# Kernel optimization log

Measured on AMD Instinct MI355X. Metric: run time of the kernel, lower is better.

Reference implementation:

```python
import jax, jax.numpy as jnp
import numpy as np

H = 1024      # hidden_size
NH = 16       # num_attention_heads
HD = H // NH  # attention_head_size = 64
FF = 4096     # intermediate_size
EPS = 1e-5


def setup_inputs() -> dict:
    key = jax.random.key(0)
    ks = jax.random.split(key, 16)
    B, S = 8, 512
    s = lambda d: 1.0 / np.sqrt(d)
    return {
        "hidden_states": jax.random.normal(ks[0], (B, S, H), jnp.float32),
        "attention_mask": jnp.zeros((B, 1, 1, S), jnp.float32),  # additive mask
        "wq": jax.random.normal(ks[1], (H, H), jnp.float32) * s(H),
        "bq": jnp.zeros((H,), jnp.float32),
        "wk": jax.random.normal(ks[2], (H, H), jnp.float32) * s(H),
        "bk": jnp.zeros((H,), jnp.float32),
        "wv": jax.random.normal(ks[3], (H, H), jnp.float32) * s(H),
        "bv": jnp.zeros((H,), jnp.float32),
        "wo": jax.random.normal(ks[4], (H, H), jnp.float32) * s(H),
        "bo": jnp.zeros((H,), jnp.float32),
        "ln1_g": jnp.ones((H,), jnp.float32),
        "ln1_b": jnp.zeros((H,), jnp.float32),
        "wi": jax.random.normal(ks[5], (H, FF), jnp.float32) * s(H),
        "bi": jnp.zeros((FF,), jnp.float32),
        "wo2": jax.random.normal(ks[6], (FF, H), jnp.float32) * s(FF),
        "bo2": jnp.zeros((H,), jnp.float32),
        "ln2_g": jnp.ones((H,), jnp.float32),
        "ln2_b": jnp.zeros((H,), jnp.float32),
    }


def _layer_norm(x, g, b):
    mu = jnp.mean(x, axis=-1, keepdims=True)
    var = jnp.mean(jnp.square(x - mu), axis=-1, keepdims=True)
    return (x - mu) * jax.lax.rsqrt(var + EPS) * g + b


def reference(hidden_states, attention_mask, wq, bq, wk, bk, wv, bv,
              wo, bo, ln1_g, ln1_b, wi, bi, wo2, bo2, ln2_g, ln2_b):
    B, S, _ = hidden_states.shape
    split = lambda x: x.reshape(B, S, NH, HD).transpose(0, 2, 1, 3)  # [B,NH,S,HD]
    q = split(hidden_states @ wq + bq)
    k = split(hidden_states @ wk + bk)
    v = split(hidden_states @ wv + bv)
    # scaled dot-product attention with additive mask (dropout = eval identity)
    scores = jnp.einsum("bhqd,bhkd->bhqk", q, k) / np.sqrt(HD)
    scores = scores + attention_mask
    probs = jax.nn.softmax(scores, axis=-1)
    ctx = jnp.einsum("bhqk,bhkd->bhqd", probs, v)
    ctx = ctx.transpose(0, 2, 1, 3).reshape(B, S, H)
    # RobertaSelfOutput: dense + residual + LayerNorm
    attn_out = _layer_norm(ctx @ wo + bo + hidden_states, ln1_g, ln1_b)
    # FFN: intermediate (gelu) + output dense + residual + LayerNorm
    inter = jax.nn.gelu(attn_out @ wi + bi, approximate=False)
    layer_out = _layer_norm(inter @ wo2 + bo2 + attn_out, ln2_g, ln2_b)
    return layer_out
```

## Files before the change

### kernel.cpp

```cpp
#include <hip/hip_runtime.h>
#include <math.h>

#define DI __device__ __forceinline__

typedef unsigned short u16;
typedef __attribute__((ext_vector_type(8))) u16 u16x8;
typedef __attribute__((ext_vector_type(4))) u16 u16x4;
typedef __attribute__((ext_vector_type(8))) __bf16 bf16x8;
typedef __attribute__((ext_vector_type(4))) float f32x4;

typedef const __attribute__((address_space(1))) unsigned int g_u32;
typedef __attribute__((address_space(3))) unsigned int l_u32;

DI float bf2f(u16 u) {
  unsigned v = ((unsigned)u) << 16;
  float f; __builtin_memcpy(&f, &v, 4); return f;
}
DI u16 f2bf(float f) {
  unsigned u; __builtin_memcpy(&u, &f, 4);
  u += 0x7fff + ((u >> 16) & 1);
  return (u16)(u >> 16);
}
DI f32x4 mfma16(bf16x8 a, bf16x8 b, f32x4 c) {
  return __builtin_amdgcn_mfma_f32_16x16x32_bf16(a, b, c, 0, 0, 0);
}
DI void gl16(const void* g, const u16* lds) {
  __builtin_amdgcn_global_load_lds((g_u32*)g, (l_u32*)lds, 16, 0, 0);
}
DI unsigned cvtpk(float lo, float hi) {
  unsigned d;
  asm("v_cvt_pk_bf16_f32 %0, %1, %2" : "=v"(d) : "v"(lo), "v"(hi));
  return d;
}

__global__ __launch_bounds__(256) void cvt_bf16_k(const float* __restrict__ in,
                                                  u16* __restrict__ out, int n) {
  int i = (blockIdx.x * 256 + threadIdx.x) * 8;
  if (i >= n) return;
  float4 a = *(const float4*)(in + i);
  float4 b = *(const float4*)(in + i + 4);
  u16x8 o;
  o[0] = f2bf(a.x); o[1] = f2bf(a.y); o[2] = f2bf(a.z); o[3] = f2bf(a.w);
  o[4] = f2bf(b.x); o[5] = f2bf(b.y); o[6] = f2bf(b.z); o[7] = f2bf(b.w);
  *(u16x8*)(out + i) = o;
}

__global__ __launch_bounds__(256) void tcvt_k(const float* __restrict__ in,
                                              u16* __restrict__ out, int K, int N) {
  __shared__ float tile[32][33];
  int n0 = blockIdx.x * 32, k0 = blockIdx.y * 32;
  int tx = threadIdx.x & 31, ty = threadIdx.x >> 5;
  #pragma unroll
  for (int i = 0; i < 4; i++) {
    int kr = ty + i * 8;
    tile[kr][tx] = in[(size_t)(k0 + kr) * N + n0 + tx];
  }
  __syncthreads();
  #pragma unroll
  for (int i = 0; i < 4; i++) {
    int nr = ty + i * 8;
    out[(size_t)(n0 + nr) * K + k0 + tx] = f2bf(tile[tx][nr]);
  }
}

__global__ __launch_bounds__(256) void pack_bias_k(const float* __restrict__ b0,
                                                   const float* __restrict__ b1,
                                                   const float* __restrict__ b2,
                                                   float* __restrict__ out) {
  int i = blockIdx.x * 256 + threadIdx.x;
  float v = (i < 1024) ? b0[i] : (i < 2048 ? b1[i - 1024] : b2[i - 2048]);
  out[i] = v;
}

__global__ __launch_bounds__(256) void vtr_k(const u16* __restrict__ QKV,
                                             u16* __restrict__ VT) {
  __shared__ u16 tile[64][72];
  const int t = threadIdx.x;
  const int kt = blockIdx.x, bh = blockIdx.y;
  const int b = bh >> 4, h = bh & 15;
  {
    int r = t >> 2, d0 = (t & 3) * 16;
    const u16* src = &QKV[((size_t)(b * 512 + kt * 64 + r)) * 3072 + 2048 + h * 64 + d0];
    *(u16x8*)&tile[r][d0] = *(const u16x8*)src;
    *(u16x8*)&tile[r][d0 + 8] = *(const u16x8*)(src + 8);
  }
  __syncthreads();
  int d = t >> 2, kseg = (t & 3) * 16;
  u16x8 o0, o1;
  #pragma unroll
  for (int j = 0; j < 8; j++) { o0[j] = tile[kseg + j][d]; o1[j] = tile[kseg + 8 + j][d]; }
  u16* dst = &VT[((size_t)bh << 15) + (size_t)d * 512 + kt * 64 + kseg];
  *(u16x8*)dst = o0;
  *(u16x8*)(dst + 8) = o1;
}

#define QUAD(d, mh, nh) do {                                                          \
  const u16* Ab_ = &sA[d][wr][0];                                                     \
  const u16* Bb_ = &sB[d][wc >> 1][0];                                                \
  bf16x8 af_[4][2], bv_[2][2];                                                        \
  _Pragma("unroll") for (int i_ = 0; i_ < 4; i_++) {                                  \
    int row_ = (mh) * 64 + i_ * 16 + r15;                                             \
    _Pragma("unroll") for (int ks_ = 0; ks_ < 2; ks_++)                               \
      af_[i_][ks_] = *(const bf16x8*)&Ab_[row_ * 64 + ((((ks_ << 2) | kg) + row_) & 7) * 8]; } \
  _Pragma("unroll") for (int j_ = 0; j_ < 2; j_++) {                                  \
    int row_ = (wc & 1) * 64 + (nh) * 32 + j_ * 16 + r15;                             \
    _Pragma("unroll") for (int ks_ = 0; ks_ < 2; ks_++)                               \
      bv_[j_][ks_] = *(const bf16x8*)&Bb_[row_ * 64 + ((((ks_ << 2) | kg) + row_) & 7) * 8]; } \
  __builtin_amdgcn_s_barrier();                                                       \
  __builtin_amdgcn_s_setprio(1);                                                      \
  _Pragma("unroll") for (int i_ = 0; i_ < 4; i_++)                                    \
    _Pragma("unroll") for (int j_ = 0; j_ < 2; j_++)                                  \
      _Pragma("unroll") for (int ks_ = 0; ks_ < 2; ks_++)                             \
        acc[(mh) * 4 + i_][(nh) * 2 + j_] =                                           \
            mfma16(af_[i_][ks_], bv_[j_][ks_], acc[(mh) * 4 + i_][(nh) * 2 + j_]);    \
  __builtin_amdgcn_s_setprio(0);                                                      \
} while (0)

template<int EPI, int SPLITK>
__global__ __launch_bounds__(512, 2) void gemm8p_k(const u16* __restrict__ A,
                                                   const u16* __restrict__ Bt,
                                                   const float* __restrict__ bias,
                                                   void* __restrict__ out,
                                                   int M, int N, int K) {
  __shared__ __align__(16) u16 sA[2][2][128 * 64];
  __shared__ __align__(16) u16 sB[2][2][128 * 64];
  const int tid = threadIdx.x;
  const int lane = tid & 63, wid = tid >> 6;
  const int wr = wid >> 2, wc = wid & 3;
  const int r15 = lane & 15, kg = lane >> 4;

  const int GX = gridDim.x, GY = gridDim.y;
  int nwg = GX * GY;
  int orig = blockIdx.y * GX + blockIdx.x;
  int s = (orig & 7) * (nwg >> 3) + (orig >> 3);
  int bx = s / GY, by = s - bx * GY;
  const int bm = by * 256, bn = bx * 256;

  const int z = blockIdx.z;
  int tilesK = K >> 6;
  int qs = tilesK / SPLITK, rs = tilesK - qs * SPLITK;
  int ntz = qs + (z < rs ? 1 : 0);
  int k0 = (z * qs + (z < rs ? z : rs)) << 6;

  f32x4 acc[8][4];
  #pragma unroll
  for (int i = 0; i < 8; i++)
    #pragma unroll
    for (int j = 0; j < 4; j++) acc[i][j] = (f32x4){0.f, 0.f, 0.f, 0.f};

  const int drw = tid >> 3;
  const int gsl8 = ((tid - drw) & 7) << 3;
  const u16* pA0 = A  + (size_t)(bm +       drw) * K + k0 + gsl8;
  const u16* pA1 = A  + (size_t)(bm + 128 + drw) * K + k0 + gsl8;
  const u16* pB0 = Bt + (size_t)(bn +       drw) * K + k0 + gsl8;
  const u16* pB1 = Bt + (size_t)(bn + 128 + drw) * K + k0 + gsl8;
  const size_t s2o = (size_t)64 * K;
  const int dld = wid << 9;

  auto stageTile = [&](int d) {
    u16* dA0 = &sA[d][0][dld]; u16* dA1 = &sA[d][1][dld];
    u16* dB0 = &sB[d][0][dld]; u16* dB1 = &sB[d][1][dld];
    gl16(pA0, dA0); gl16(pA0 + s2o, dA0 + 4096);
    gl16(pB0, dB0); gl16(pB0 + s2o, dB0 + 4096);
    gl16(pA1, dA1); gl16(pA1 + s2o, dA1 + 4096);
    gl16(pB1, dB1); gl16(pB1 + s2o, dB1 + 4096);
    pA0 += 64; pA1 += 64; pB0 += 64; pB1 += 64;
  };

  stageTile(0);
  if (ntz > 1) stageTile(1);

  for (int t = 0; t < ntz; ++t) {
    int d = t & 1;
    if (t + 1 < ntz) asm volatile("s_waitcnt vmcnt(8)" ::: "memory");
    else             asm volatile("s_waitcnt vmcnt(0)" ::: "memory");
    __builtin_amdgcn_s_barrier();
    QUAD(d, 0, 0);
    QUAD(d, 0, 1);
    QUAD(d, 1, 0);
    QUAD(d, 1, 1);
    __builtin_amdgcn_s_barrier();
    __builtin_amdgcn_sched_barrier(0);
    if (t + 2 < ntz) stageTile(d);
  }

  #pragma unroll
  for (int ii = 0; ii < 8; ii++) {
    int row = bm + wr * 128 + ii * 16 + kg * 4;
    #pragma unroll
    for (int jj = 0; jj < 4; jj++) {
      int col = bn + wc * 64 + jj * 16 + r15;
      if (EPI == 4) {
        size_t zoff = (size_t)z * M * N;
        #pragma unroll
        for (int q2 = 0; q2 < 4; q2++)
          ((float*)out)[zoff + (size_t)(row + q2) * N + col] = acc[ii][jj][q2];
      } else {
        float bv = bias[col];
        #pragma unroll
        for (int q2 = 0; q2 < 4; q2++) {
          float v = acc[ii][jj][q2] + bv;
          if (EPI == 2) v = 0.5f * v * (1.0f + erff(v * 0.70710678118f));
          ((u16*)out)[(size_t)(row + q2) * N + col] = f2bf(v);
        }
      }
    }
  }
}

template<int EPI>
__global__ __launch_bounds__(256) void gemm_bt_k(const u16* __restrict__ A,
                                                 const u16* __restrict__ Bt,
                                                 const float* __restrict__ bias,
                                                 const void* __restrict__ resid,
                                                 u16* __restrict__ out,
                                                 int M, int N, int K) {
  __shared__ __align__(16) u16 As[2][128 * 64];
  __shared__ __align__(16) u16 Bs[2][128 * 64];
  const int tid = threadIdx.x;
  const int lane = tid & 63, wid = tid >> 6;
  const int wm = (wid >> 1) * 64, wn = (wid & 1) * 64;
  const int r15 = lane & 15, kg = lane >> 4;
  const int srow = lane >> 3;

  const int GX = gridDim.x, GY = gridDim.y;
  int nwg = GX * GY;
  int orig = blockIdx.y * GX + blockIdx.x;
  int s = (orig & 7) * (nwg >> 3) + (orig >> 3);
  int bx = s / GY, by = s - bx * GY;
  const int bm = by * 128, bn = bx * 128;

  f32x4 acc[4][4];
  #pragma unroll
  for (int i = 0; i < 4; i++)
    #pragma unroll
    for (int j = 0; j < 4; j++) acc[i][j] = (f32x4){0.f, 0.f, 0.f, 0.f};

  const u16* pAc[4]; const u16* pBc[4];
  #pragma unroll
  for (int c = 0; c < 4; c++) {
    int chunk = (c << 2) | wid;
    int row = (chunk << 3) + srow;
    int gsl = ((lane & 7) - row) & 7;
    pAc[c] = A  + (size_t)(bm + row) * K + (gsl << 3);
    pBc[c] = Bt + (size_t)(bn + row) * K + (gsl << 3);
  }
  auto STAGE = [&](int buf, int kt) {
    #pragma unroll
    for (int c = 0; c < 4; c++) {
      int chunk = (c << 2) | wid;
      gl16(pAc[c] + kt, &As[buf][chunk << 9]);
      gl16(pBc[c] + kt, &Bs[buf][chunk << 9]);
    }
  };
  auto COMPUTE = [&](int buf) {
    #pragma unroll
    for (int ks = 0; ks < 2; ks++) {
      bf16x8 af[4], bfr[4];
      #pragma unroll
      for (int i = 0; i < 4; i++) {
        int row = wm + i * 16 + r15;
        af[i] = *(const bf16x8*)&As[buf][row * 64 + (((ks << 2) + kg + row) & 7) * 8];
      }
      #pragma unroll
      for (int i = 0; i < 4; i++) {
        int row = wn + i * 16 + r15;
        bfr[i] = *(const bf16x8*)&Bs[buf][row * 64 + (((ks << 2) + kg + row) & 7) * 8];
      }
      #pragma unroll
      for (int i = 0; i < 4; i++)
        #pragma unroll
        for (int j = 0; j < 4; j++)
          acc[i][j] = mfma16(af[i], bfr[j], acc[i][j]);
    }
  };

  const int nt = K >> 6;
  STAGE(0, 0);
  if (nt > 1) STAGE(1, 64);
  for (int t = 0; t < nt; ++t) {
    if (t + 1 < nt) asm volatile("s_waitcnt vmcnt(8)" ::: "memory");
    else            asm volatile("s_waitcnt vmcnt(0)" ::: "memory");
    __builtin_amdgcn_s_barrier();
    COMPUTE(t & 1);
    __builtin_amdgcn_s_barrier();
    __builtin_amdgcn_sched_barrier(0);
    if (t + 2 < nt) STAGE(t & 1, (t + 2) << 6);
  }

  #pragma unroll
  for (int i = 0; i < 4; i++) {
    int row0 = bm + wm + i * 16 + kg * 4;
    #pragma unroll
    for (int j = 0; j < 4; j++) {
      int col = bn + wn + j * 16 + r15;
      float bv = bias[col];
      #pragma unroll
      for (int q2 = 0; q2 < 4; q2++) {
        int row = row0 + q2;
        float v = acc[i][j][q2] + bv;
        if (EPI == 1) v += ((const float*)resid)[(size_t)row * N + col];
        out[(size_t)row * N + col] = f2bf(v);
      }
    }
  }
}

__global__ __launch_bounds__(256) void fattn_k(const u16* __restrict__ QKV,
                                               const u16* __restrict__ VT,
                                               const float* __restrict__ mask,
                                               u16* __restrict__ ctx) {
  __shared__ __align__(16) u16 sK[2][64 * 64];
  __shared__ __align__(16) u16 sV[2][64 * 64];
  __shared__ float sMask[512];
  const int t = threadIdx.x, lane = t & 63, wid = t >> 6;
  const int q15 = lane & 15, g = lane >> 4;
  const int qb = blockIdx.x, h = blockIdx.y, b = blockIdx.z;
  const int bh = b * 16 + h;
  const int qrow0 = qb * 128 + wid * 32;

  if (t < 128) *(float4*)&sMask[t * 4] = *(const float4*)&mask[b * 512 + t * 4];

  bf16x8 qf[2][2];
  #pragma unroll
  for (int qt = 0; qt < 2; qt++)
    #pragma unroll
    for (int c = 0; c < 2; c++)
      qf[qt][c] = *(const bf16x8*)&QKV[(size_t)(b * 512 + qrow0 + qt * 16 + q15) * 3072 +
                                       h * 64 + c * 32 + g * 8];

  const int srow0 = t >> 3;
  const int ssl = (((t & 7) - (t >> 3)) & 7) << 3;
  const u16* pK = QKV + (size_t)(b * 512 + srow0) * 3072 + 1024 + h * 64 + ssl;
  const u16* pV = VT + ((size_t)bh << 15) + (size_t)srow0 * 512 + ssl;
  const size_t kS2 = (size_t)32 * 3072;
  const size_t vS2 = (size_t)32 * 512;
  const int dld = t * 8;

  auto stage = [&](int d) {
    gl16(pK, &sK[d][dld]); gl16(pK + kS2, &sK[d][dld + 2048]);
    gl16(pV, &sV[d][dld]); gl16(pV + vS2, &sV[d][dld + 2048]);
    pK += 64 * 3072; pV += 64;
  };

  stage(0); stage(1);

  float m_[2] = {-1e30f, -1e30f}, l_[2] = {0.f, 0.f};
  f32x4 oacc[2][4];
  #pragma unroll
  for (int qt = 0; qt < 2; qt++)
    #pragma unroll
    for (int dt = 0; dt < 4; dt++) oacc[qt][dt] = (f32x4){0.f, 0.f, 0.f, 0.f};

  const int bp0 = ((g & 1) * 32 + q15) * 4;
  const int bp1 = bp0 + 64;

  for (int kt = 0; kt < 8; ++kt) {
    const int d = kt & 1;
    if (kt < 7) asm volatile("s_waitcnt vmcnt(4)" ::: "memory");
    else        asm volatile("s_waitcnt vmcnt(0)" ::: "memory");
    __builtin_amdgcn_s_barrier();

    f32x4 sc[2][4];
    #pragma unroll
    for (int qt = 0; qt < 2; qt++)
      #pragma unroll
      for (int k16 = 0; k16 < 4; k16++) sc[qt][k16] = (f32x4){0.f, 0.f, 0.f, 0.f};
    #pragma unroll
    for (int k16 = 0; k16 < 4; k16++) {
      int row = k16 * 16 + q15;
      bf16x8 ak0 = *(const bf16x8*)&sK[d][row * 64 + ((g + row) & 7) * 8];
      bf16x8 ak1 = *(const bf16x8*)&sK[d][row * 64 + ((4 + g + row) & 7) * 8];
      #pragma unroll
      for (int qt = 0; qt < 2; qt++) {
        sc[qt][k16] = mfma16(ak0, qf[qt][0], sc[qt][k16]);
        sc[qt][k16] = mfma16(ak1, qf[qt][1], sc[qt][k16]);
      }
    }

    float mk[4][4];
    #pragma unroll
    for (int k16 = 0; k16 < 4; k16++)
      #pragma unroll
      for (int r = 0; r < 4; r++)
        mk[k16][r] = sMask[kt * 64 + k16 * 16 + g * 4 + r];
    float p[2][16];
    #pragma unroll
    for (int qt = 0; qt < 2; qt++)
      #pragma unroll
      for (int k16 = 0; k16 < 4; k16++)
        #pragma unroll
        for (int r = 0; r < 4; r++)
          p[qt][k16 * 4 + r] = sc[qt][k16][r] * 0.125f + mk[k16][r];

    #pragma unroll
    for (int qt = 0; qt < 2; qt++) {
      float tmax = p[qt][0];
      #pragma unroll
      for (int j = 1; j < 16; j++) tmax = fmaxf(tmax, p[qt][j]);
      tmax = fmaxf(tmax, __shfl_xor(tmax, 16));
      tmax = fmaxf(tmax, __shfl_xor(tmax, 32));
      float mn = fmaxf(m_[qt], tmax);
      float al = __expf(m_[qt] - mn);
      m_[qt] = mn;
      float ts = 0.f;
      #pragma unroll
      for (int j = 0; j < 16; j++) { p[qt][j] = __expf(p[qt][j] - mn); ts += p[qt][j]; }
      ts += __shfl_xor(ts, 16);
      ts += __shfl_xor(ts, 32);
      l_[qt] = l_[qt] * al + ts;
      #pragma unroll
      for (int r = 0; r < 4; r++) {
        float alq = __shfl(al, g * 4 + r);
        #pragma unroll
        for (int dt = 0; dt < 4; dt++) oacc[qt][dt][r] *= alq;
      }
    }

    unsigned dwp[2][4][2];
    #pragma unroll
    for (int qt = 0; qt < 2; qt++)
      #pragma unroll
      for (int k16 = 0; k16 < 4; k16++) {
        dwp[qt][k16][0] = cvtpk(p[qt][k16 * 4 + 0], p[qt][k16 * 4 + 1]);
        dwp[qt][k16][1] = cvtpk(p[qt][k16 * 4 + 2], p[qt][k16 * 4 + 3]);
      }

    #pragma unroll
    for (int cp = 0; cp < 2; cp++) {
      bf16x8 pa[2];
      #pragma unroll
      for (int qt = 0; qt < 2; qt++) {
        union { unsigned u[4]; bf16x8 v; } pu;
        #pragma unroll
        for (int pp = 0; pp < 2; pp++) {
          unsigned a0 = __builtin_amdgcn_ds_bpermute(bp0, (int)dwp[qt][2 * cp][pp]);
          unsigned b0 = __builtin_amdgcn_ds_bpermute(bp0, (int)dwp[qt][2 * cp + 1][pp]);
          unsigned a1 = __builtin_amdgcn_ds_bpermute(bp1, (int)dwp[qt][2 * cp][pp]);
          unsigned b1 = __builtin_amdgcn_ds_bpermute(bp1, (int)dwp[qt][2 * cp + 1][pp]);
          pu.u[pp] = (g & 2) ? b0 : a0;
          pu.u[2 + pp] = (g & 2) ? b1 : a1;
        }
        pa[qt] = pu.v;
      }
      #pragma unroll
      for (int dt = 0; dt < 4; dt++) {
        int row = dt * 16 + q15;
        bf16x8 vf = *(const bf16x8*)&sV[d][row * 64 + (((cp << 2) + g + row) & 7) * 8];
        oacc[0][dt] = mfma16(pa[0], vf, oacc[0][dt]);
        oacc[1][dt] = mfma16(pa[1], vf, oacc[1][dt]);
      }
    }

    __builtin_amdgcn_s_barrier();
    __builtin_amdgcn_sched_barrier(0);
    if (kt + 2 < 8) stage(d);
  }

  #pragma unroll
  for (int qt = 0; qt < 2; qt++) {
    float linv[4];
    #pragma unroll
    for (int r = 0; r < 4; r++) linv[r] = 1.0f / __shfl(l_[qt], g * 4 + r);
    #pragma unroll
    for (int dt = 0; dt < 4; dt++)
      #pragma unroll
      for (int r = 0; r < 4; r++) {
        int row = qrow0 + qt * 16 + g * 4 + r;
        ctx[(size_t)(b * 512 + row) * 1024 + h * 64 + dt * 16 + q15] =
            f2bf(oacc[qt][dt][r] * linv[r]);
      }
  }
}

template<int OUTF32>
__global__ __launch_bounds__(256) void ln_k(const u16* __restrict__ in,
                                            const float* __restrict__ g,
                                            const float* __restrict__ be,
                                            void* __restrict__ out) {
  int row = blockIdx.x, t = threadIdx.x;
  const u16* rp = in + (size_t)row * 1024 + t * 4;
  u16x4 raw = *(const u16x4*)rp;
  float x[4];
  #pragma unroll
  for (int i = 0; i < 4; i++) x[i] = bf2f(raw[i]);
  float s = x[0] + x[1] + x[2] + x[3];
  float q = x[0]*x[0] + x[1]*x[1] + x[2]*x[2] + x[3]*x[3];
  #pragma unroll
  for (int off = 32; off; off >>= 1) {
    s += __shfl_down(s, off);
    q += __shfl_down(q, off);
  }
  __shared__ float rs_[4], rq_[4];
  int wid = t >> 6, lane = t & 63;
  if (!lane) { rs_[wid] = s; rq_[wid] = q; }
  __syncthreads();
  float S1 = rs_[0] + rs_[1] + rs_[2] + rs_[3];
  float S2 = rq_[0] + rq_[1] + rq_[2] + rq_[3];
  float mu = S1 * (1.0f / 1024.0f);
  float inv = rsqrtf(S2 * (1.0f / 1024.0f) - mu * mu + 1e-5f);
  #pragma unroll
  for (int i = 0; i < 4; i++) {
    int c = t * 4 + i;
    float y = (x[i] - mu) * inv * g[c] + be[c];
    if (OUTF32) ((float*)out)[(size_t)row * 1024 + c] = y;
    else        ((u16*)out)[(size_t)row * 1024 + c] = f2bf(y);
  }
}

__global__ __launch_bounds__(256) void ln2r_k(const float* __restrict__ part,
                                              const float* __restrict__ bias,
                                              const u16* __restrict__ resid,
                                              const float* __restrict__ g,
                                              const float* __restrict__ be,
                                              float* __restrict__ out) {
  const int row = blockIdx.x, t = threadIdx.x;
  const size_t base = (size_t)row * 1024 + t * 4;
  float4 p0 = *(const float4*)(part + base);
  float4 p1 = *(const float4*)(part + 4194304 + base);
  float4 p2 = *(const float4*)(part + 8388608 + base);
  u16x4 rr = *(const u16x4*)(resid + base);
  float x[4];
  x[0] = p0.x + p1.x + p2.x + bias[t*4+0] + bf2f(rr[0]);
  x[1] = p0.y + p1.y + p2.y + bias[t*4+1] + bf2f(rr[1]);
  x[2] = p0.z + p1.z + p2.z + bias[t*4+2] + bf2f(rr[2]);
  x[3] = p0.w + p1.w + p2.w + bias[t*4+3] + bf2f(rr[3]);
  float s = x[0] + x[1] + x[2] + x[3];
  float q = x[0]*x[0] + x[1]*x[1] + x[2]*x[2] + x[3]*x[3];
  #pragma unroll
  for (int off = 32; off; off >>= 1) {
    s += __shfl_down(s, off);
    q += __shfl_down(q, off);
  }
  __shared__ float rs_[4], rq_[4];
  int wid = t >> 6, lane = t & 63;
  if (!lane) { rs_[wid] = s; rq_[wid] = q; }
  __syncthreads();
  float S1 = rs_[0] + rs_[1] + rs_[2] + rs_[3];
  float S2 = rq_[0] + rq_[1] + rq_[2] + rq_[3];
  float mu = S1 * (1.0f / 1024.0f);
  float inv = rsqrtf(S2 * (1.0f / 1024.0f) - mu * mu + 1e-5f);
  #pragma unroll
  for (int i = 0; i < 4; i++) {
    int c = t * 4 + i;
    out[(size_t)row * 1024 + c] = (x[i] - mu) * inv * g[c] + be[c];
  }
}

extern "C" void kernel_launch(void* const* d_in, const int* in_sizes, int n_in,
                              void* d_out, int out_size, void* d_ws, size_t ws_size,
                              hipStream_t stream) {
  const float* hidden = (const float*)d_in[0];
  const float* mask   = (const float*)d_in[1];
  const float* wq  = (const float*)d_in[2];  const float* bq  = (const float*)d_in[3];
  const float* wk  = (const float*)d_in[4];  const float* bk  = (const float*)d_in[5];
  const float* wv  = (const float*)d_in[6];  const float* bv  = (const float*)d_in[7];
  const float* wo  = (const float*)d_in[8];  const float* bo  = (const float*)d_in[9];
  const float* ln1g = (const float*)d_in[10]; const float* ln1b = (const float*)d_in[11];
  const float* wi  = (const float*)d_in[12]; const float* bi  = (const float*)d_in[13];
  const float* wo2 = (const float*)d_in[14]; const float* bo2 = (const float*)d_in[15];
  const float* ln2g = (const float*)d_in[16]; const float* ln2b = (const float*)d_in[17];

  char* ws = (char*)d_ws;
  u16*   WqkvT = (u16*)(ws + 0);
  u16*   WoT   = (u16*)(ws + 6291456);
  u16*   Xb    = (u16*)(ws + 8388608);
  u16*   VTb   = (u16*)(ws + 8388608);
  u16*   QKVb  = (u16*)(ws + 16777216);
  u16*   Ctx   = (u16*)(ws + 41943040);
  u16*   AD    = (u16*)(ws + 50331648);
  float* part  = (float*)(ws + 0);
  u16*   AO    = (u16*)(ws + 58720256);
  u16*   Inter = (u16*)(ws + 67108864);
  u16*   WiT   = (u16*)(ws + 100663296);
  u16*   Wo2T  = (u16*)(ws + 109051904);
  float* bqkv  = (float*)(ws + 117440512);

  cvt_bf16_k<<<2048, 256, 0, stream>>>(hidden, Xb, 4194304);
  tcvt_k<<<dim3(32, 32),  256, 0, stream>>>(wq,  WqkvT,                1024, 1024);
  tcvt_k<<<dim3(32, 32),  256, 0, stream>>>(wk,  WqkvT + 1024 * 1024,  1024, 1024);
  tcvt_k<<<dim3(32, 32),  256, 0, stream>>>(wv,  WqkvT + 2048 * 1024,  1024, 1024);
  tcvt_k<<<dim3(32, 32),  256, 0, stream>>>(wo,  WoT,  1024, 1024);
  tcvt_k<<<dim3(128, 32), 256, 0, stream>>>(wi,  WiT,  1024, 4096);
  tcvt_k<<<dim3(32, 128), 256, 0, stream>>>(wo2, Wo2T, 4096, 1024);
  pack_bias_k<<<12, 256, 0, stream>>>(bq, bk, bv, bqkv);

  gemm8p_k<0, 1><<<dim3(12, 16, 1), 512, 0, stream>>>(Xb, WqkvT, bqkv, QKVb, 4096, 3072, 1024);

  vtr_k<<<dim3(8, 128), 256, 0, stream>>>(QKVb, VTb);

  fattn_k<<<dim3(4, 16, 8), 256, 0, stream>>>(QKVb, VTb, mask, Ctx);

  gemm_bt_k<1><<<dim3(8, 32), 256, 0, stream>>>(Ctx, WoT, bo, hidden, AD, 4096, 1024, 1024);
  ln_k<0><<<4096, 256, 0, stream>>>(AD, ln1g, ln1b, AO);

  gemm8p_k<2, 1><<<dim3(16, 16, 1), 512, 0, stream>>>(AO, WiT, bi, Inter, 4096, 4096, 1024);

  gemm8p_k<4, 3><<<dim3(4, 16, 3), 512, 0, stream>>>(Inter, Wo2T, nullptr, part, 4096, 1024, 4096);

  ln2r_k<<<4096, 256, 0, stream>>>(part, bo2, AO, ln2g, ln2b, (float*)d_out);
}
```

Before: 374.2 us.

## Interleave per-half global prefetch with MFMA phases in 256x256 GEMM

Restructures the 8-wave GEMM main loop so each wave computes a checkerboard of A/B halves. The global-to-LDS loads for the next k-tile are issued in four quarter-tile chunks, interleaved between the four MFMA phases with finer vmcnt waits. This replaces the old whole-tile double-buffer refill at the end of each iteration. It also changes the warp-to-output mapping so A fragments can be reused across phases, which cuts LDS reads. The intent is better overlap of memory traffic with matrix math, at the cost of more barriers and tighter waitcnt ordering that could introduce hazards.

After: 388.2 us. +3.7%, slower.

```diff
diff --git a/kernel.cpp b/kernel.cpp
--- a/kernel.cpp
+++ b/kernel.cpp
@@ -94,25 +94,24 @@
   *(u16x8*)(dst + 8) = o1;
 }
 
-#define QUAD(d, mh, nh) do {                                                          \
-  const u16* Ab_ = &sA[d][wr][0];                                                     \
-  const u16* Bb_ = &sB[d][wc >> 1][0];                                                \
-  bf16x8 af_[4][2], bv_[2][2];                                                        \
+#define LD_A(half) do { const u16* Ah_ = &sA[d][half][0];                             \
   _Pragma("unroll") for (int i_ = 0; i_ < 4; i_++) {                                  \
-    int row_ = (mh) * 64 + i_ * 16 + r15;                                             \
+    int row_ = wr * 64 + i_ * 16 + r15;                                               \
     _Pragma("unroll") for (int ks_ = 0; ks_ < 2; ks_++)                               \
-      af_[i_][ks_] = *(const bf16x8*)&Ab_[row_ * 64 + ((((ks_ << 2) | kg) + row_) & 7) * 8]; } \
+      afr[i_][ks_] = *(const bf16x8*)&Ah_[row_ * 64 + (((ks_ * 4 + kg) + row_) & 7) * 8]; } \
+} while (0)
+#define LD_B(half) do { const u16* Bh_ = &sB[d][half][0];                             \
   _Pragma("unroll") for (int j_ = 0; j_ < 2; j_++) {                                  \
-    int row_ = (wc & 1) * 64 + (nh) * 32 + j_ * 16 + r15;                             \
+    int row_ = wc * 32 + j_ * 16 + r15;                                               \
     _Pragma("unroll") for (int ks_ = 0; ks_ < 2; ks_++)                               \
-      bv_[j_][ks_] = *(const bf16x8*)&Bb_[row_ * 64 + ((((ks_ << 2) | kg) + row_) & 7) * 8]; } \
-  __builtin_amdgcn_s_barrier();                                                       \
-  __builtin_amdgcn_s_setprio(1);                                                      \
+      bvr[j_][ks_] = *(const bf16x8*)&Bh_[row_ * 64 + (((ks_ * 4 + kg) + row_) & 7) * 8]; } \
+} while (0)
+#define MFMA_PH(ah, bh) do { __builtin_amdgcn_s_setprio(1);                           \
   _Pragma("unroll") for (int i_ = 0; i_ < 4; i_++)                                    \
     _Pragma("unroll") for (int j_ = 0; j_ < 2; j_++)                                  \
       _Pragma("unroll") for (int ks_ = 0; ks_ < 2; ks_++)                             \
-        acc[(mh) * 4 + i_][(nh) * 2 + j_] =                                           \
-            mfma16(af_[i_][ks_], bv_[j_][ks_], acc[(mh) * 4 + i_][(nh) * 2 + j_]);    \
+        acc[(ah) * 4 + i_][(bh) * 2 + j_] =                                           \
+            mfma16(afr[i_][ks_], bvr[j_][ks_], acc[(ah) * 4 + i_][(bh) * 2 + j_]);    \
   __builtin_amdgcn_s_setprio(0);                                                      \
 } while (0)
 
@@ -157,55 +156,67 @@
   const size_t s2o = (size_t)64 * K;
   const int dld = wid << 9;
 
-  auto stageTile = [&](int d) {
-    u16* dA0 = &sA[d][0][dld]; u16* dA1 = &sA[d][1][dld];
-    u16* dB0 = &sB[d][0][dld]; u16* dB1 = &sB[d][1][dld];
-    gl16(pA0, dA0); gl16(pA0 + s2o, dA0 + 4096);
-    gl16(pB0, dB0); gl16(pB0 + s2o, dB0 + 4096);
-    gl16(pA1, dA1); gl16(pA1 + s2o, dA1 + 4096);
-    gl16(pB1, dB1); gl16(pB1 + s2o, dB1 + 4096);
-    pA0 += 64; pA1 += 64; pB0 += 64; pB1 += 64;
-  };
-
-  stageTile(0);
-  if (ntz > 1) stageTile(1);
+  auto stA0 = [&](int d) { u16* D = &sA[d][0][dld]; gl16(pA0, D); gl16(pA0 + s2o, D + 4096); pA0 += 64; };
+  auto stB0 = [&](int d) { u16* D = &sB[d][0][dld]; gl16(pB0, D); gl16(pB0 + s2o, D + 4096); pB0 += 64; };
+  auto stA1 = [&](int d) { u16* D = &sA[d][1][dld]; gl16(pA1, D); gl16(pA1 + s2o, D + 4096); pA1 += 64; };
+  auto stB1 = [&](int d) { u16* D = &sB[d][1][dld]; gl16(pB1, D); gl16(pB1 + s2o, D + 4096); pB1 += 64; };
+
+  stA0(0); stB0(0); stA1(0); stB1(0);
 
   for (int t = 0; t < ntz; ++t) {
-    int d = t & 1;
-    if (t + 1 < ntz) asm volatile("s_waitcnt vmcnt(8)" ::: "memory");
-    else             asm volatile("s_waitcnt vmcnt(0)" ::: "memory");
+    const int d = t & 1;
+    const bool pf = (t + 1 < ntz);
+    bf16x8 afr[4][2], bvr[2][2];
+
+    asm volatile("s_waitcnt vmcnt(4)" ::: "memory");
+    asm volatile("s_waitcnt lgkmcnt(0)" ::: "memory");
+    __builtin_amdgcn_sched_barrier(0);
     __builtin_amdgcn_s_barrier();
-    QUAD(d, 0, 0);
-    QUAD(d, 0, 1);
-    QUAD(d, 1, 0);
-    QUAD(d, 1, 1);
+    if (pf) stA0(d ^ 1);
+    LD_A(0); LD_B(0);
+    MFMA_PH(0, 0);
+    if (pf) { asm volatile("s_waitcnt vmcnt(4)" ::: "memory"); stB0(d ^ 1); }
+    else    { asm volatile("s_waitcnt vmcnt(2)" ::: "memory"); }
     __builtin_amdgcn_s_barrier();
-    __builtin_amdgcn_sched_barrier(0);
-    if (t + 2 < ntz) stageTile(d);
-  }
-
-  #pragma unroll
-  for (int ii = 0; ii < 8; ii++) {
-    int row = bm + wr * 128 + ii * 16 + kg * 4;
-    #pragma unroll
-    for (int jj = 0; jj < 4; jj++) {
-      int col = bn + wc * 64 + jj * 16 + r15;
-      if (EPI == 4) {
-        size_t zoff = (size_t)z * M * N;
+    LD_A(1);
+    MFMA_PH(1, 0);
+    if (pf) { asm volatile("s_waitcnt vmcnt(4)" ::: "memory"); stA1(d ^ 1); }
+    else    { asm volatile("s_waitcnt vmcnt(0)" ::: "memory"); }
+    __builtin_amdgcn_s_barrier();
+    LD_B(1);
+    MFMA_PH(1, 1);
+    if (pf) stB1(d ^ 1);
+    LD_A(0);
+    MFMA_PH(0, 1);
+  }
+
+  #pragma unroll
+  for (int ah = 0; ah < 2; ah++)
+    #pragma unroll
+    for (int ii = 0; ii < 4; ii++) {
+      int row = bm + ah * 128 + wr * 64 + ii * 16 + kg * 4;
+      #pragma unroll
+      for (int bh = 0; bh < 2; bh++)
         #pragma unroll
-        for (int q2 = 0; q2 < 4; q2++)
-          ((float*)out)[zoff + (size_t)(row + q2) * N + col] = acc[ii][jj][q2];
-      } else {
-        float bv = bias[col];
-        #pragma unroll
-        for (int q2 = 0; q2 < 4; q2++) {
-          float v = acc[ii][jj][q2] + bv;
-          if (EPI == 2) v = 0.5f * v * (1.0f + erff(v * 0.70710678118f));
-          ((u16*)out)[(size_t)(row + q2) * N + col] = f2bf(v);
+        for (int jj = 0; jj < 2; jj++) {
+          int col = bn + bh * 128 + wc * 32 + jj * 16 + r15;
+          f32x4 av = acc[ah * 4 + ii][bh * 2 + jj];
+          if (EPI == 4) {
+            size_t zoff = (size_t)z * M * N;
+            #pragma unroll
+            for (int q2 = 0; q2 < 4; q2++)
+              ((float*)out)[zoff + (size_t)(row + q2) * N + col] = av[q2];
+          } else {
+            float bv = bias[col];
+            #pragma unroll
+            for (int q2 = 0; q2 < 4; q2++) {
+              float v = av[q2] + bv;
+              if (EPI == 2) v = 0.5f * v * (1.0f + erff(v * 0.70710678118f));
+              ((u16*)out)[(size_t)(row + q2) * N + col] = f2bf(v);
+            }
+          }
         }
-      }
     }
-  }
 }
 
 template<int EPI>
```
